# Optimization experiments

Hardware: AMD Instinct MI355X
Metric: run time of the kernel (lower is better)

The kernel has to match this reference:

```python
import jax, jax.numpy as jnp
import numpy as np

DIM, NUM_HEADS, WINDOW = 1024, 16, 256
HEAD_DIM = DIM // NUM_HEADS
B, L = 2, 2048


def rotate_half(x):
    x1, x2 = jnp.split(x, 2, axis=-1)
    return jnp.concatenate([-x2, x1], axis=-1)


def setup_inputs() -> dict:
    key = jax.random.key(0)
    kx, kq, kk, kv, ko = jax.random.split(key, 5)
    x = jax.random.normal(kx, (B, L, DIM), dtype=jnp.float32)
    # realistic RoPE tables (L, head_dim)
    inv_freq = 1.0 / (10000.0 ** (np.arange(0, HEAD_DIM, 2, dtype=np.float32) / HEAD_DIM))
    ang = np.arange(L, dtype=np.float32)[:, None] * inv_freq[None, :]  # (L, hd/2)
    ang = np.concatenate([ang, ang], axis=-1)  # (L, hd)
    cos = jnp.asarray(np.cos(ang))
    sin = jnp.asarray(np.sin(ang))
    scale = 1.0 / np.sqrt(DIM)
    Wq = jax.random.normal(kq, (DIM, DIM), dtype=jnp.float32) * scale
    Wk = jax.random.normal(kk, (DIM, DIM), dtype=jnp.float32) * scale
    Wv = jax.random.normal(kv, (DIM, DIM), dtype=jnp.float32) * scale
    Wo = jax.random.normal(ko, (DIM, DIM), dtype=jnp.float32) * scale
    return {"x": x, "cos": cos, "sin": sin, "Wq": Wq, "Wk": Wk, "Wv": Wv, "Wo": Wo}


def reference(x, cos, sin, Wq, Wk, Wv, Wo):
    Bx, Lx, D = x.shape
    H, hd, w = NUM_HEADS, HEAD_DIM, WINDOW
    q = (x @ Wq.T).reshape(Bx, Lx, H, hd)
    k = (x @ Wk.T).reshape(Bx, Lx, H, hd)
    v = (x @ Wv.T).reshape(Bx, Lx, H, hd)
    c = cos[None, :, None, :]  # broadcast over batch, heads
    s = sin[None, :, None, :]
    q = q * c + rotate_half(q) * s
    k = k * c + rotate_half(k) * s
    # (B, H, L, hd)
    q = q.transpose(0, 2, 1, 3)
    k = k.transpose(0, 2, 1, 3)
    v = v.transpose(0, 2, 1, 3)
    i = jnp.arange(Lx)[:, None]
    j = jnp.arange(Lx)[None, :]
    # causal & within sliding window: i - w <= j <= i
    mask = (j <= i) & (j >= i - w)
    scores = jnp.einsum("bhqd,bhkd->bhqk", q, k) / jnp.sqrt(jnp.asarray(hd, x.dtype))
    scores = jnp.where(mask[None, None], scores, jnp.finfo(scores.dtype).min)
    attn = jax.nn.softmax(scores, axis=-1)
    out = jnp.einsum("bhqk,bhkd->bhqd", attn, v)
    out = out.transpose(0, 2, 1, 3).reshape(Bx, Lx, D)
    return out @ Wo.T
```

## Files before the change

### kernel.cpp

```cpp
#include <hip/hip_runtime.h>

#define DIM 1024
#define NH  16
#define HD  64
#define BB  2
#define LL  2048
#define WIN 256
#define MM  (BB * LL)
#define NQKV (3 * DIM)
#define SEG  (DIM * DIM)

typedef __bf16 bf16x8 __attribute__((ext_vector_type(8)));
typedef float  f32x4  __attribute__((ext_vector_type(4)));
typedef unsigned short u16x8 __attribute__((ext_vector_type(8)));

__device__ __forceinline__ unsigned short f2bf(float f) {
    union { float f; unsigned int i; } v; v.f = f;
    unsigned int r = v.i + 0x7fffu + ((v.i >> 16) & 1u);
    return (unsigned short)(r >> 16);
}
__device__ __forceinline__ bf16x8 load8bf(const unsigned short* p) {
    uint4 u = *reinterpret_cast<const uint4*>(p);
    return __builtin_bit_cast(bf16x8, u);
}
__device__ __forceinline__ void gll16(const void* g, void* l) {
    __builtin_amdgcn_global_load_lds(
        (const __attribute__((address_space(1))) unsigned int*)g,
        (__attribute__((address_space(3))) unsigned int*)l, 16, 0, 0);
}

__global__ __launch_bounds__(256) void convert_inputs(
    const float* __restrict__ x,
    const float* __restrict__ Wq, const float* __restrict__ Wk,
    const float* __restrict__ Wv, const float* __restrict__ Wo,
    unsigned short* __restrict__ xb,
    unsigned short* __restrict__ wqkv,
    unsigned short* __restrict__ wob)
{
    const int y = blockIdx.y;
    const size_t base = ((size_t)blockIdx.x * 256 + threadIdx.x) * 8;
    const float* src; unsigned short* dst;
    if (y < 4)       { src = x + (size_t)y * SEG;  dst = xb + (size_t)y * SEG; }
    else if (y == 4) { src = Wq; dst = wqkv; }
    else if (y == 5) { src = Wk; dst = wqkv + SEG; }
    else if (y == 6) { src = Wv; dst = wqkv + 2 * (size_t)SEG; }
    else             { src = Wo; dst = wob; }
    float4 a = ((const float4*)(src + base))[0];
    float4 b = ((const float4*)(src + base))[1];
    u16x8 r;
    r[0] = f2bf(a.x); r[1] = f2bf(a.y); r[2] = f2bf(a.z); r[3] = f2bf(a.w);
    r[4] = f2bf(b.x); r[5] = f2bf(b.y); r[6] = f2bf(b.z); r[7] = f2bf(b.w);
    *(u16x8*)(dst + base) = r;
}

__global__ __launch_bounds__(256, 4) void qkv_gemm(
    const unsigned short* __restrict__ xb,
    const unsigned short* __restrict__ wqkv,
    const float* __restrict__ cosb, const float* __restrict__ sinb,
    unsigned short* __restrict__ qws, unsigned short* __restrict__ kws,
    unsigned short* __restrict__ vT)
{
    __shared__ __align__(16) unsigned short smem[2 * 128 * 64];
    unsigned short* As = smem;
    unsigned short* Bs = smem + 128 * 64;
    const int t = threadIdx.x;
    const int lane = t & 63, w = t >> 6;
    const int wm = w >> 1, wn = w & 1;
    const int lr = lane & 15, quad = lane >> 4;

    const int id   = blockIdx.y * 24 + blockIdx.x;
    const int xcd  = id & 7, slot = id >> 3;
    const int bxn  = (xcd & 1) * 12 + (slot % 12);
    const int byn  = (xcd >> 1) * 8 + (slot / 12);
    const int n0 = bxn * 128, m0 = byn * 128;

    f32x4 acc[4][4];
    for (int i = 0; i < 4; i++) for (int j = 0; j < 4; j++) acc[i][j] = 0.0f;

    const int rsub = t >> 3;
    const int csw  = (t & 7) ^ (rsub & 7);
    const int sw7  = lr & 7;

    for (int k0 = 0; k0 < DIM; k0 += 64) {
        __syncthreads();
        #pragma unroll
        for (int p = 0; p < 4; p++) {
            const int row = p * 32 + rsub;
            gll16(xb   + (size_t)(m0 + row) * DIM + k0 + csw * 8,
                  &As[p * 2048 + t * 8]);
            gll16(wqkv + (size_t)(n0 + row) * DIM + k0 + csw * 8,
                  &Bs[p * 2048 + t * 8]);
        }
        __syncthreads();
        #pragma unroll
        for (int kk = 0; kk < 2; kk++) {
            bf16x8 af[4], bfr[4];
            #pragma unroll
            for (int mi = 0; mi < 4; mi++) {
                const int R = wm * 64 + mi * 16 + lr;
                af[mi] = load8bf(&As[R * 64 + (((kk * 4 + quad) ^ sw7) * 8)]);
            }
            #pragma unroll
            for (int ni = 0; ni < 4; ni++) {
                const int R = wn * 64 + ni * 16 + lr;
                bfr[ni] = load8bf(&Bs[R * 64 + (((kk * 4 + quad) ^ sw7) * 8)]);
            }
            #pragma unroll
            for (int mi = 0; mi < 4; mi++)
                #pragma unroll
                for (int ni = 0; ni < 4; ni++)
                    acc[mi][ni] = __builtin_amdgcn_mfma_f32_16x16x32_bf16(
                        af[mi], bfr[ni], acc[mi][ni], 0, 0, 0);
        }
    }

    const int ng = n0 + wn * 64;
    const int which = ng >> 10;
    const int h = (ng & (DIM - 1)) >> 6;

    if (which == 2) {
        __syncthreads();
        unsigned short* T = smem + w * 2048;
        const int token0 = m0 + wm * 64;
        const int b  = token0 >> 11;
        const int lg = (token0 & (LL - 1)) + (lane & 7) * 8;
        #pragma unroll
        for (int p = 0; p < 2; p++) {
            #pragma unroll
            for (int ni = 2 * p; ni < 2 * p + 2; ni++) {
                const int dl = (ni & 1) * 16 + lr;
                const int g4 = (dl & 7) << 2;
                #pragma unroll
                for (int mi = 0; mi < 4; mi++)
                    #pragma unroll
                    for (int reg = 0; reg < 4; reg++) {
                        const int l = mi * 16 + quad * 4 + reg;
                        const int cw = (l >> 1) ^ g4;
                        T[dl * 64 + cw * 2 + (l & 1)] = f2bf(acc[mi][ni][reg]);
                    }
            }
            #pragma unroll
            for (int s = 0; s < 4; s++) {
                const int dl = s * 8 + (lane >> 3);
                const int d  = p * 32 + dl;
                const int g4 = (dl & 7) << 2;
                const int pd = ((lane & 7) * 4) ^ g4;
                uint4 val = *(const uint4*)&T[dl * 64 + pd * 2];
                *(uint4*)&vT[((size_t)(b * NH + h) * HD + d) * LL + lg] = val;
            }
        }
    } else {
        unsigned short* dst = (which == 0) ? qws : kws;
        #pragma unroll
        for (int mi = 0; mi < 4; mi++) {
            #pragma unroll
            for (int reg = 0; reg < 4; reg++) {
                const int row = m0 + wm * 64 + mi * 16 + quad * 4 + reg;
                const int b = row >> 11, l = row & (LL - 1);
                #pragma unroll
                for (int ni = 0; ni < 4; ni++) {
                    const int d = ni * 16 + lr;
                    const float c = cosb[l * HD + d];
                    const float s = sinb[l * HD + d];
                    const float partner = (d < 32) ? -acc[mi][ni + 2][reg]
                                                   :  acc[mi][ni - 2][reg];
                    dst[((size_t)(b * NH + h) * LL + l) * HD + d] =
                        f2bf(acc[mi][ni][reg] * c + partner * s);
                }
            }
        }
    }
}

#define SW_SPAN 384
#define PSTR 40
__global__ __launch_bounds__(512, 4) void swa_attn(
    const unsigned short* __restrict__ qws,
    const unsigned short* __restrict__ kws,
    const unsigned short* __restrict__ vT,
    unsigned short* __restrict__ aout)
{
    __shared__ __align__(16) unsigned short Ks[SW_SPAN * 64];
    __shared__ __align__(16) unsigned short Pc[8][2][16][PSTR];

    const int t = threadIdx.x;
    const int lane = t & 63, w = t >> 6;

    const int id   = (blockIdx.z * NH + blockIdx.y) * 16 + blockIdx.x;
    const int xcd  = id & 7, slot = id >> 3;
    const int hb   = xcd * 4 + (slot >> 4);
    const int qb   = slot & 15;
    const int h = hb & 15, b = hb >> 4;

    const int q0 = qb * 128;
    const int base_key = q0 - WIN;

    const int lr = lane & 15, quad = lane >> 4, ko = quad * 8;
    const size_t base = ((size_t)(b * NH + h)) * LL * HD;
    const unsigned short* Q  = qws + base;
    const unsigned short* K  = kws + base;
    const unsigned short* VT = vT + base;

    {
        const int rsub = t >> 3;
        const int csw  = (t & 7) ^ (rsub & 7);
        #pragma unroll
        for (int p = 0; p < 6; p++) {
            const int j = min(max(base_key + p * 64 + rsub, 0), LL - 1);
            gll16(K + (size_t)j * HD + csw * 8, &Ks[p * 4096 + t * 8]);
        }
    }
    const int i0 = q0 + w * 16;
    const int wkey = i0 - WIN;
    const bf16x8 qa0 = load8bf(Q + (size_t)(i0 + lr) * HD + ko);
    const bf16x8 qa1 = load8bf(Q + (size_t)(i0 + lr) * HD + 32 + ko);
    __syncthreads();

    float rowsum[4] = {0.f, 0.f, 0.f, 0.f};
    f32x4 o[4];
    #pragma unroll
    for (int nt = 0; nt < 4; nt++) o[nt] = 0.0f;

    if (q0 >= WIN) {
        bool mlo[4], mhi[4];
        #pragma unroll
        for (int reg = 0; reg < 4; reg++) {
            mlo[reg] = (lr >= quad * 4 + reg);
            mhi[reg] = (lr <= quad * 4 + reg);
        }
        #pragma unroll
        for (int kc = 0; kc < 9; kc++) {
            const int pb = kc & 1;
            {
                const int kt = 2 * kc;
                const int R = w * 16 + kt * 16 + lr;
                const bf16x8 kb0 = load8bf(&Ks[R * 64 + ((quad       ^ (R & 7)) * 8)]);
                const bf16x8 kb1 = load8bf(&Ks[R * 64 + (((quad + 4) ^ (R & 7)) * 8)]);
                f32x4 s = 0.0f;
                s = __builtin_amdgcn_mfma_f32_16x16x32_bf16(qa0, kb0, s, 0, 0, 0);
                s = __builtin_amdgcn_mfma_f32_16x16x32_bf16(qa1, kb1, s, 0, 0, 0);
                #pragma unroll
                for (int reg = 0; reg < 4; reg++) {
                    float e = __expf(s[reg] * 0.125f);
                    if (kt == 0)  e = mlo[reg] ? e : 0.0f;
                    if (kt == 16) e = mhi[reg] ? e : 0.0f;
                    rowsum[reg] += e;
                    Pc[w][pb][quad * 4 + reg][lr] = f2bf(e);
                }
            }
            bf16x8 bv[4];
            {
                int kb = wkey + kc * 32 + ko;
                kb = min(kb, LL - 8);
                #pragma unroll
                for (int nt = 0; nt < 4; nt++)
                    bv[nt] = load8bf(VT + (size_t)(nt * 16 + lr) * LL + kb);
            }
            {
                const int kt = 2 * kc + 1;
                if (kt > 16) {
                    #pragma unroll
                    for (int reg = 0; reg < 4; reg++)
                        Pc[w][pb][quad * 4 + reg][16 + lr] = 0;
                } else {
                    const int R = w * 16 + kt * 16 + lr;
                    const bf16x8 kb0 = load8bf(&Ks[R * 64 + ((quad       ^ (R & 7)) * 8)]);
                    const bf16x8 kb1 = load8bf(&Ks[R * 64 + (((quad + 4) ^ (R & 7)) * 8)]);
                    f32x4 s = 0.0f;
                    s = __builtin_amdgcn_mfma_f32_16x16x32_bf16(qa0, kb0, s, 0, 0, 0);
                    s = __builtin_amdgcn_mfma_f32_16x16x32_bf16(qa1, kb1, s, 0, 0, 0);
                    #pragma unroll
                    for (int reg = 0; reg < 4; reg++) {
                        const float e = __expf(s[reg] * 0.125f);
                        rowsum[reg] += e;
                        Pc[w][pb][quad * 4 + reg][16 + lr] = f2bf(e);
                    }
                }
            }
            const bf16x8 pa = load8bf(&Pc[w][pb][lr][ko]);
            #pragma unroll
            for (int nt = 0; nt < 4; nt++)
                o[nt] = __builtin_amdgcn_mfma_f32_16x16x32_bf16(pa, bv[nt], o[nt], 0, 0, 0);
        }
    } else {
        #pragma unroll
        for (int kc = 0; kc < 9; kc++) {
            const int pb = kc & 1;
            #pragma unroll
            for (int sub = 0; sub < 2; sub++) {
                const int kt = 2 * kc + sub;
                const int R = min(w * 16 + kt * 16 + lr, SW_SPAN - 1);
                const bf16x8 kb0 = load8bf(&Ks[R * 64 + ((quad       ^ (R & 7)) * 8)]);
                const bf16x8 kb1 = load8bf(&Ks[R * 64 + (((quad + 4) ^ (R & 7)) * 8)]);
                f32x4 s = 0.0f;
                s = __builtin_amdgcn_mfma_f32_16x16x32_bf16(qa0, kb0, s, 0, 0, 0);
                s = __builtin_amdgcn_mfma_f32_16x16x32_bf16(qa1, kb1, s, 0, 0, 0);
                #pragma unroll
                for (int reg = 0; reg < 4; reg++) {
                    const int i = i0 + quad * 4 + reg;
                    const int j = wkey + kt * 16 + lr;
                    const bool valid = (j >= 0) && (j <= i) && (j >= i - WIN);
                    const float e = valid ? __expf(s[reg] * 0.125f) : 0.0f;
                    rowsum[reg] += e;
                    Pc[w][pb][quad * 4 + reg][sub * 16 + lr] = f2bf(e);
                }
            }
            const bf16x8 pa = load8bf(&Pc[w][pb][lr][ko]);
            int kb = wkey + kc * 32 + ko;
            kb = min(max(kb, 0), LL - 8);
            bf16x8 bv[4];
            #pragma unroll
            for (int nt = 0; nt < 4; nt++)
                bv[nt] = load8bf(VT + (size_t)(nt * 16 + lr) * LL + kb);
            #pragma unroll
            for (int nt = 0; nt < 4; nt++)
                o[nt] = __builtin_amdgcn_mfma_f32_16x16x32_bf16(pa, bv[nt], o[nt], 0, 0, 0);
        }
    }

    float inv[4];
    #pragma unroll
    for (int reg = 0; reg < 4; reg++) {
        float s = rowsum[reg];
        s += __shfl_xor(s, 1); s += __shfl_xor(s, 2);
        s += __shfl_xor(s, 4); s += __shfl_xor(s, 8);
        inv[reg] = 1.0f / s;
    }

    #pragma unroll
    for (int nt = 0; nt < 4; nt++) {
        #pragma unroll
        for (int reg = 0; reg < 4; reg++) {
            const int i = i0 + quad * 4 + reg;
            const int d = nt * 16 + lr;
            aout[((size_t)(b * LL + i)) * DIM + h * HD + d] =
                f2bf(o[nt][reg] * inv[reg]);
        }
    }
}

__global__ __launch_bounds__(256, 4) void out_gemm(
    const unsigned short* __restrict__ A,
    const unsigned short* __restrict__ Wob,
    float* __restrict__ out)
{
    __shared__ __align__(16) unsigned short smem[64 * 64 + 64 * 64];
    unsigned short* As = smem;
    unsigned short* Bs = smem + 64 * 64;
    const int t = threadIdx.x;
    const int lane = t & 63, w = t >> 6;
    const int wm = w >> 1, wn = w & 1;
    const int lr = lane & 15, quad = lane >> 4;

    const int id   = blockIdx.y * 16 + blockIdx.x;
    const int xcd  = id & 7, slot = id >> 3;
    const int bx   = (xcd & 1) * 8 + (slot & 7);
    const int by   = (xcd >> 1) * 16 + (slot >> 3);
    const int n0 = bx * 64, m0 = by * 64;

    f32x4 acc[2][2];
    for (int i = 0; i < 2; i++) for (int j = 0; j < 2; j++) acc[i][j] = 0.0f;

    const int rsub = t >> 3;
    const int csw  = (t & 7) ^ (rsub & 7);
    const int sw7  = lr & 7;

    for (int k0 = 0; k0 < DIM; k0 += 64) {
        __syncthreads();
        #pragma unroll
        for (int p = 0; p < 2; p++) {
            const int row = p * 32 + rsub;
            gll16(A   + (size_t)(m0 + row) * DIM + k0 + csw * 8,
                  &As[p * 2048 + t * 8]);
            gll16(Wob + (size_t)(n0 + row) * DIM + k0 + csw * 8,
                  &Bs[p * 2048 + t * 8]);
        }
        __syncthreads();
        #pragma unroll
        for (int kk = 0; kk < 2; kk++) {
            bf16x8 af[2], bfr[2];
            #pragma unroll
            for (int mi = 0; mi < 2; mi++) {
                const int R = wm * 32 + mi * 16 + lr;
                af[mi] = load8bf(&As[R * 64 + (((kk * 4 + quad) ^ sw7) * 8)]);
            }
            #pragma unroll
            for (int ni = 0; ni < 2; ni++) {
                const int R = wn * 32 + ni * 16 + lr;
                bfr[ni] = load8bf(&Bs[R * 64 + (((kk * 4 + quad) ^ sw7) * 8)]);
            }
            #pragma unroll
            for (int mi = 0; mi < 2; mi++)
                #pragma unroll
                for (int ni = 0; ni < 2; ni++)
                    acc[mi][ni] = __builtin_amdgcn_mfma_f32_16x16x32_bf16(
                        af[mi], bfr[ni], acc[mi][ni], 0, 0, 0);
        }
    }

    #pragma unroll
    for (int mi = 0; mi < 2; mi++) {
        #pragma unroll
        for (int reg = 0; reg < 4; reg++) {
            const int row = m0 + wm * 32 + mi * 16 + quad * 4 + reg;
            #pragma unroll
            for (int ni = 0; ni < 2; ni++) {
                const int col = n0 + wn * 32 + ni * 16 + lr;
                out[(size_t)row * DIM + col] = acc[mi][ni][reg];
            }
        }
    }
}

extern "C" void kernel_launch(void* const* d_in, const int* in_sizes, int n_in,
                              void* d_out, int out_size, void* d_ws, size_t ws_size,
                              hipStream_t stream)
{
    const float* x    = (const float*)d_in[0];
    const float* cosb = (const float*)d_in[1];
    const float* sinb = (const float*)d_in[2];
    const float* Wq   = (const float*)d_in[3];
    const float* Wk   = (const float*)d_in[4];
    const float* Wv   = (const float*)d_in[5];
    const float* Wo   = (const float*)d_in[6];
    float* out = (float*)d_out;

    unsigned short* xb   = (unsigned short*)d_ws;
    unsigned short* wqkv = xb + (size_t)MM * DIM;
    unsigned short* wob  = wqkv + (size_t)NQKV * DIM;
    unsigned short* qws  = wob + (size_t)DIM * DIM;
    unsigned short* kws  = qws + (size_t)BB * NH * LL * HD;
    unsigned short* vT   = kws + (size_t)BB * NH * LL * HD;
    unsigned short* aws  = xb;

    convert_inputs<<<dim3(SEG / (256 * 8), 8), 256, 0, stream>>>(
        x, Wq, Wk, Wv, Wo, xb, wqkv, wob);
    qkv_gemm<<<dim3(NQKV / 128, MM / 128), 256, 0, stream>>>(
        xb, wqkv, cosb, sinb, qws, kws, vT);
    swa_attn<<<dim3(LL / 128, NH, BB), 512, 0, stream>>>(qws, kws, vT, aws);
    out_gemm<<<dim3(DIM / 64, MM / 64), 256, 0, stream>>>(aws, wob, out);
}
```

Before: 157.6 us.

## Pass attention probabilities through register shuffles instead of LDS staging buffer

Swaps the QK^T MFMA operands so each lane holds scores for one query row, then packs the exp values to bf16 and rearranges them into the PV A-operand layout with cross-lane shuffles, replacing the Pc shared-memory round trip. The row-sum reduction is reworked to match the transposed layout, V loads are issued earlier in each iteration, and s_setprio brackets the MFMA groups. It removes LDS writes, reads and their ordering cost, in exchange for eight shuffles plus selects per chunk.

Result: no change. 158.5 us (+0.6%).

```diff
diff --git a/kernel.cpp b/kernel.cpp
--- a/kernel.cpp
+++ b/kernel.cpp
@@ -27,6 +27,9 @@
     __builtin_amdgcn_global_load_lds(
         (const __attribute__((address_space(1))) unsigned int*)g,
         (__attribute__((address_space(3))) unsigned int*)l, 16, 0, 0);
+}
+__device__ __forceinline__ unsigned pack2bf(float lo, float hi) {
+    return (unsigned)f2bf(lo) | ((unsigned)f2bf(hi) << 16);
 }
 
 __global__ __launch_bounds__(256) void convert_inputs(
@@ -173,7 +176,6 @@
 }
 
 #define SW_SPAN 384
-#define PSTR 40
 __global__ __launch_bounds__(512, 4) void swa_attn(
     const unsigned short* __restrict__ qws,
     const unsigned short* __restrict__ kws,
@@ -181,7 +183,6 @@
     unsigned short* __restrict__ aout)
 {
     __shared__ __align__(16) unsigned short Ks[SW_SPAN * 64];
-    __shared__ __align__(16) unsigned short Pc[8][2][16][PSTR];
 
     const int t = threadIdx.x;
     const int lane = t & 63, w = t >> 6;
@@ -216,76 +217,106 @@
     const bf16x8 qa1 = load8bf(Q + (size_t)(i0 + lr) * HD + 32 + ko);
     __syncthreads();
 
-    float rowsum[4] = {0.f, 0.f, 0.f, 0.f};
+    float rowsumL = 0.f;
     f32x4 o[4];
     #pragma unroll
     for (int nt = 0; nt < 4; nt++) o[nt] = 0.0f;
 
+    const int srcA = (quad & 1) * 32 + lr;
+    const int srcB = srcA + 16;
+    const bool useB = (quad >= 2);
+
     if (q0 >= WIN) {
-        bool mlo[4], mhi[4];
-        #pragma unroll
-        for (int reg = 0; reg < 4; reg++) {
-            mlo[reg] = (lr >= quad * 4 + reg);
-            mhi[reg] = (lr <= quad * 4 + reg);
-        }
         #pragma unroll
         for (int kc = 0; kc < 9; kc++) {
-            const int pb = kc & 1;
+            bf16x8 bv[4];
+            {
+                int kb = wkey + kc * 32 + ko;
+                kb = min(kb, LL - 8);
+                #pragma unroll
+                for (int nt = 0; nt < 4; nt++)
+                    bv[nt] = load8bf(VT + (size_t)(nt * 16 + lr) * LL + kb);
+            }
+            unsigned L0, H0, L1, H1;
             {
                 const int kt = 2 * kc;
                 const int R = w * 16 + kt * 16 + lr;
                 const bf16x8 kb0 = load8bf(&Ks[R * 64 + ((quad       ^ (R & 7)) * 8)]);
                 const bf16x8 kb1 = load8bf(&Ks[R * 64 + (((quad + 4) ^ (R & 7)) * 8)]);
                 f32x4 s = 0.0f;
-                s = __builtin_amdgcn_mfma_f32_16x16x32_bf16(qa0, kb0, s, 0, 0, 0);
-                s = __builtin_amdgcn_mfma_f32_16x16x32_bf16(qa1, kb1, s, 0, 0, 0);
+                __builtin_amdgcn_s_setprio(1);
+                s = __builtin_amdgcn_mfma_f32_16x16x32_bf16(kb0, qa0, s, 0, 0, 0);
+                s = __builtin_amdgcn_mfma_f32_16x16x32_bf16(kb1, qa1, s, 0, 0, 0);
+                __builtin_amdgcn_s_setprio(0);
+                float e[4];
                 #pragma unroll
                 for (int reg = 0; reg < 4; reg++) {
-                    float e = __expf(s[reg] * 0.125f);
-                    if (kt == 0)  e = mlo[reg] ? e : 0.0f;
-                    if (kt == 16) e = mhi[reg] ? e : 0.0f;
-                    rowsum[reg] += e;
-                    Pc[w][pb][quad * 4 + reg][lr] = f2bf(e);
+                    const int qk = quad * 4 + reg;
+                    float ee = __expf(s[reg] * 0.125f);
+                    if (kt == 0)  ee = (qk >= lr) ? ee : 0.0f;
+                    if (kt == 16) ee = (qk <= lr) ? ee : 0.0f;
+                    rowsumL += ee;
+                    e[reg] = ee;
                 }
-            }
-            bf16x8 bv[4];
-            {
-                int kb = wkey + kc * 32 + ko;
-                kb = min(kb, LL - 8);
-                #pragma unroll
-                for (int nt = 0; nt < 4; nt++)
-                    bv[nt] = load8bf(VT + (size_t)(nt * 16 + lr) * LL + kb);
+                L0 = pack2bf(e[0], e[1]); H0 = pack2bf(e[2], e[3]);
             }
             {
                 const int kt = 2 * kc + 1;
                 if (kt > 16) {
-                    #pragma unroll
-                    for (int reg = 0; reg < 4; reg++)
-                        Pc[w][pb][quad * 4 + reg][16 + lr] = 0;
+                    L1 = 0u; H1 = 0u;
                 } else {
                     const int R = w * 16 + kt * 16 + lr;
                     const bf16x8 kb0 = load8bf(&Ks[R * 64 + ((quad       ^ (R & 7)) * 8)]);
                     const bf16x8 kb1 = load8bf(&Ks[R * 64 + (((quad + 4) ^ (R & 7)) * 8)]);
                     f32x4 s = 0.0f;
-                    s = __builtin_amdgcn_mfma_f32_16x16x32_bf16(qa0, kb0, s, 0, 0, 0);
-                    s = __builtin_amdgcn_mfma_f32_16x16x32_bf16(qa1, kb1, s, 0, 0, 0);
+                    __builtin_amdgcn_s_setprio(1);
+                    s = __builtin_amdgcn_mfma_f32_16x16x32_bf16(kb0, qa0, s, 0, 0, 0);
+                    s = __builtin_amdgcn_mfma_f32_16x16x32_bf16(kb1, qa1, s, 0, 0, 0);
+                    __builtin_amdgcn_s_setprio(0);
+                    float e[4];
                     #pragma unroll
                     for (int reg = 0; reg < 4; reg++) {
-                        const float e = __expf(s[reg] * 0.125f);
-                        rowsum[reg] += e;
-                        Pc[w][pb][quad * 4 + reg][16 + lr] = f2bf(e);
+                        const float ee = __expf(s[reg] * 0.125f);
+                        rowsumL += ee;
+                        e[reg] = ee;
                     }
+                    L1 = pack2bf(e[0], e[1]); H1 = pack2bf(e[2], e[3]);
                 }
             }
-            const bf16x8 pa = load8bf(&Pc[w][pb][lr][ko]);
-            #pragma unroll
-            for (int nt = 0; nt < 4; nt++)
-                o[nt] = __builtin_amdgcn_mfma_f32_16x16x32_bf16(pa, bv[nt], o[nt], 0, 0, 0);
+            {
+                const int a0 = __shfl((int)L0, srcA);
+                const int a1 = __shfl((int)H0, srcA);
+                const int a2 = __shfl((int)L0, srcB);
+                const int a3 = __shfl((int)H0, srcB);
+                const int b0 = __shfl((int)L1, srcA);
+                const int b1 = __shfl((int)H1, srcA);
+                const int b2 = __shfl((int)L1, srcB);
+                const int b3 = __shfl((int)H1, srcB);
+                uint4 w4;
+                w4.x = (unsigned)(useB ? b0 : a0);
+                w4.y = (unsigned)(useB ? b1 : a1);
+                w4.z = (unsigned)(useB ? b2 : a2);
+                w4.w = (unsigned)(useB ? b3 : a3);
+                const bf16x8 pa = __builtin_bit_cast(bf16x8, w4);
+                __builtin_amdgcn_s_setprio(1);
+                #pragma unroll
+                for (int nt = 0; nt < 4; nt++)
+                    o[nt] = __builtin_amdgcn_mfma_f32_16x16x32_bf16(pa, bv[nt], o[nt], 0, 0, 0);
+                __builtin_amdgcn_s_setprio(0);
+            }
         }
     } else {
         #pragma unroll
         for (int kc = 0; kc < 9; kc++) {
-            const int pb = kc & 1;
+            bf16x8 bv[4];
+            {
+                int kb = wkey + kc * 32 + ko;
+                kb = min(max(kb, 0), LL - 8);
+                #pragma unroll
+                for (int nt = 0; nt < 4; nt++)
+                    bv[nt] = load8bf(VT + (size_t)(nt * 16 + lr) * LL + kb);
+            }
+            unsigned LH[2][2];
             #pragma unroll
             for (int sub = 0; sub < 2; sub++) {
                 const int kt = 2 * kc + sub;
@@ -293,39 +324,51 @@
                 const bf16x8 kb0 = load8bf(&Ks[R * 64 + ((quad       ^ (R & 7)) * 8)]);
                 const bf16x8 kb1 = load8bf(&Ks[R * 64 + (((quad + 4) ^ (R & 7)) * 8)]);
                 f32x4 s = 0.0f;
-                s = __builtin_amdgcn_mfma_f32_16x16x32_bf16(qa0, kb0, s, 0, 0, 0);
-                s = __builtin_amdgcn_mfma_f32_16x16x32_bf16(qa1, kb1, s, 0, 0, 0);
+                s = __builtin_amdgcn_mfma_f32_16x16x32_bf16(kb0, qa0, s, 0, 0, 0);
+                s = __builtin_amdgcn_mfma_f32_16x16x32_bf16(kb1, qa1, s, 0, 0, 0);
+                float e[4];
                 #pragma unroll
                 for (int reg = 0; reg < 4; reg++) {
-                    const int i = i0 + quad * 4 + reg;
-                    const int j = wkey + kt * 16 + lr;
+                    const int qk = quad * 4 + reg;
+                    const int i = i0 + lr;
+                    const int j = wkey + kt * 16 + qk;
                     const bool valid = (j >= 0) && (j <= i) && (j >= i - WIN);
-                    const float e = valid ? __expf(s[reg] * 0.125f) : 0.0f;
-                    rowsum[reg] += e;
-                    Pc[w][pb][quad * 4 + reg][sub * 16 + lr] = f2bf(e);
+                    const float ee = valid ? __expf(s[reg] * 0.125f) : 0.0f;
+                    rowsumL += ee;
+                    e[reg] = ee;
                 }
-            }
-            const bf16x8 pa = load8bf(&Pc[w][pb][lr][ko]);
-            int kb = wkey + kc * 32 + ko;
-            kb = min(max(kb, 0), LL - 8);
-            bf16x8 bv[4];
-            #pragma unroll
-            for (int nt = 0; nt < 4; nt++)
-                bv[nt] = load8bf(VT + (size_t)(nt * 16 + lr) * LL + kb);
-            #pragma unroll
-            for (int nt = 0; nt < 4; nt++)
-                o[nt] = __builtin_amdgcn_mfma_f32_16x16x32_bf16(pa, bv[nt], o[nt], 0, 0, 0);
-        }
-    }
-
-    float inv[4];
+                LH[sub][0] = pack2bf(e[0], e[1]); LH[sub][1] = pack2bf(e[2], e[3]);
+            }
+            {
+                const int a0 = __shfl((int)LH[0][0], srcA);
+                const int a1 = __shfl((int)LH[0][1], srcA);
+                const int a2 = __shfl((int)LH[0][0], srcB);
+                const int a3 = __shfl((int)LH[0][1], srcB);
+                const int b0 = __shfl((int)LH[1][0], srcA);
+                const int b1 = __shfl((int)LH[1][1], srcA);
+                const int b2 = __shfl((int)LH[1][0], srcB);
+                const int b3 = __shfl((int)LH[1][1], srcB);
+                uint4 w4;
+                w4.x = (unsigned)(useB ? b0 : a0);
+                w4.y = (unsigned)(useB ? b1 : a1);
+                w4.z = (unsigned)(useB ? b2 : a2);
+                w4.w = (unsigned)(useB ? b3 : a3);
+                const bf16x8 pa = __builtin_bit_cast(bf16x8, w4);
+                #pragma unroll
+                for (int nt = 0; nt < 4; nt++)
+                    o[nt] = __builtin_amdgcn_mfma_f32_16x16x32_bf16(pa, bv[nt], o[nt], 0, 0, 0);
+            }
+        }
+    }
+
+    rowsumL += __shfl_xor(rowsumL, 16);
+    rowsumL += __shfl_xor(rowsumL, 32);
+    const float inv = 1.0f / rowsumL;
+
+    float invq[4];
     #pragma unroll
-    for (int reg = 0; reg < 4; reg++) {
-        float s = rowsum[reg];
-        s += __shfl_xor(s, 1); s += __shfl_xor(s, 2);
-        s += __shfl_xor(s, 4); s += __shfl_xor(s, 8);
-        inv[reg] = 1.0f / s;
-    }
+    for (int reg = 0; reg < 4; reg++)
+        invq[reg] = __shfl(inv, quad * 4 + reg);
 
     #pragma unroll
     for (int nt = 0; nt < 4; nt++) {
@@ -334,7 +377,7 @@
             const int i = i0 + quad * 4 + reg;
             const int d = nt * 16 + lr;
             aout[((size_t)(b * LL + i)) * DIM + h * HD + d] =
-                f2bf(o[nt][reg] * inv[reg]);
+                f2bf(o[nt][reg] * invq[reg]);
         }
     }
 }
```
